# Optimization experiments

Hardware: AMD Instinct MI355X
Metric: run time of the kernel (lower is better)

The kernel has to match this reference:

```python
import jax, jax.numpy as jnp
import numpy as np
import math

B, S, D, H = 2, 2048, 1024, 16
DK = D // H


def setup_inputs() -> dict:
    key = jax.random.key(0)
    ks = jax.random.split(key, 12)
    std = 1.0 / math.sqrt(D)
    inp = {
        "query": jax.random.normal(ks[0], (B, S, D), jnp.float32),
        "key_": jax.random.normal(ks[1], (B, S, D), jnp.float32),
        "value": jax.random.normal(ks[2], (B, S, D), jnp.float32),
        # causal mask: True = masked out
        "attn_mask": jnp.triu(jnp.ones((S, S), jnp.bool_), k=1),
        "w_q": jax.random.uniform(ks[3], (D, D), jnp.float32, -std, std),
        "b_q": jax.random.uniform(ks[4], (D,), jnp.float32, -std, std),
        "w_k": jax.random.uniform(ks[5], (D, D), jnp.float32, -std, std),
        "b_k": jax.random.uniform(ks[6], (D,), jnp.float32, -std, std),
        "w_v": jax.random.uniform(ks[7], (D, D), jnp.float32, -std, std),
        "b_v": jax.random.uniform(ks[8], (D,), jnp.float32, -std, std),
        "w_o": jax.random.uniform(ks[9], (D, D), jnp.float32, -std, std),
        "b_o": jax.random.uniform(ks[10], (D,), jnp.float32, -std, std),
    }
    return inp


def reference(query, key_, value, attn_mask, w_q, b_q, w_k, b_k, w_v, b_v, w_o, b_o):
    # linear projections (torch Linear: x @ W.T + b)
    q = query @ w_q.T + b_q
    k = key_ @ w_k.T + b_k
    v = value @ w_v.T + b_v
    # [B, H, S, DK]
    q = q.reshape(B, S, H, DK).transpose(0, 2, 1, 3)
    k = k.reshape(B, S, H, DK).transpose(0, 2, 1, 3)
    v = v.reshape(B, S, H, DK).transpose(0, 2, 1, 3)
    scores = jnp.einsum("bhqd,bhkd->bhqk", q, k) / jnp.sqrt(jnp.float32(DK))
    scores = jnp.where(attn_mask[None, None, :, :], -jnp.inf, scores)
    attn = jax.nn.softmax(scores, axis=-1)
    context = jnp.einsum("bhqk,bhkd->bhqd", attn, v)
    context = context.transpose(0, 2, 1, 3).reshape(B, S, D)
    return context @ w_o.T + b_o
```

## Files before the change

kernel.cpp:

```cpp
#include <hip/hip_runtime.h>

#define B_ 2
#define S_ 2048
#define D_ 1024
#define H_ 16
#define DK_ 64
#define K_ 1024

typedef __bf16 bf16x8 __attribute__((ext_vector_type(8)));
typedef __bf16 bf16x4 __attribute__((ext_vector_type(4)));
typedef float f32x4 __attribute__((ext_vector_type(4)));

#define QSCALE 0.18033688011112042f

__device__ __forceinline__ void gload16(const void* g, void* l) {
    __builtin_amdgcn_global_load_lds(
        (const __attribute__((address_space(1))) unsigned int*)g,
        (__attribute__((address_space(3))) unsigned int*)l, 16, 0, 0);
}

__device__ __forceinline__ bf16x8 cvt8f(const float* __restrict__ p) {
    f32x4 a = *reinterpret_cast<const f32x4*>(p);
    f32x4 b = *reinterpret_cast<const f32x4*>(p + 4);
    bf16x8 r;
#pragma unroll
    for (int j = 0; j < 4; ++j) { r[j] = (__bf16)a[j]; r[j + 4] = (__bf16)b[j]; }
    return r;
}

__global__ __launch_bounds__(256) void cvt_all(
    const float* __restrict__ s0, const float* __restrict__ s1, const float* __restrict__ s2,
    const float* __restrict__ s3, const float* __restrict__ s4, const float* __restrict__ s5,
    const float* __restrict__ s6,
    __bf16* __restrict__ d0, __bf16* __restrict__ d1, __bf16* __restrict__ d2,
    __bf16* __restrict__ d3, __bf16* __restrict__ d4, __bf16* __restrict__ d5,
    __bf16* __restrict__ d6)
{
    const int y = blockIdx.y;
    const float* s; __bf16* d; int n8;
    const int n8_big = (B_ * S_ * D_) / 8, n8_w = (D_ * D_) / 8;
    switch (y) {
        case 0: s = s0; d = d0; n8 = n8_big; break;
        case 1: s = s1; d = d1; n8 = n8_big; break;
        case 2: s = s2; d = d2; n8 = n8_big; break;
        case 3: s = s3; d = d3; n8 = n8_w; break;
        case 4: s = s4; d = d4; n8 = n8_w; break;
        case 5: s = s5; d = d5; n8 = n8_w; break;
        default: s = s6; d = d6; n8 = n8_w; break;
    }
    int i = blockIdx.x * 256 + threadIdx.x;
    if (i >= n8) return;
    *reinterpret_cast<bf16x8*>(d + (size_t)i * 8) = cvt8f(s + (size_t)i * 8);
}

__global__ __launch_bounds__(512, 2) void gemm_qkv8(
    const __bf16* __restrict__ qin, const __bf16* __restrict__ kin, const __bf16* __restrict__ vin,
    const __bf16* __restrict__ wq,  const __bf16* __restrict__ wk,  const __bf16* __restrict__ wv,
    const float* __restrict__ bq,   const float* __restrict__ bk,   const float* __restrict__ bv,
    __bf16* __restrict__ qo, __bf16* __restrict__ ko, __bf16* __restrict__ vto)
{
    __shared__ __attribute__((aligned(128))) char lds[8 * 16384];

    const int tid = threadIdx.x;
    const int w = tid >> 6, lane = tid & 63;
    const int l15 = lane & 15, lh = lane >> 4;
    const int wr = w >> 2, wc = w & 3;

    const int wg   = blockIdx.x;
    const int wgid = (wg & 7) * 24 + (wg >> 3);
    const int z    = wgid >> 6;
    const int rem  = wgid & 63;

    const __bf16* A; const __bf16* Bm;
    if (z == 0)      { A = qin; Bm = wq; }
    else if (z == 1) { A = kin; Bm = wk; }
    else             { A = wv;  Bm = vin; }
    int brow, bcol;
    if (z < 2) { brow = (rem & 15) * 256; bcol = (rem >> 4) * 256; }
    else       { brow = (rem & 3)  * 256; bcol = (rem >> 2) * 256; }

    const char* Ab = (const char*)A;
    const char* Bb = (const char*)Bm;
    const int abase = brow * 2048;
    const int bbase = bcol * 2048;

    int soff[2];
#pragma unroll
    for (int j = 0; j < 2; ++j) {
        const int s = j * 512 + tid;
        const int row = s >> 2, cslot = s & 3;
        const int cswz = cslot ^ (((row >> 3) & 1) << 1);
        soff[j] = row * 2048 + cswz * 16;
    }

    auto stageHT = [&](int g, int slot) {
        const int u = g >> 2, kind = g & 3;
        const char* src = (kind & 1) ? Bb : Ab;
        const int base = ((kind & 1) ? bbase : abase) + u * 128 + (kind >> 1) * 64;
#pragma unroll
        for (int j = 0; j < 2; ++j) {
            const int ldst = __builtin_amdgcn_readfirstlane(slot * 16384 + j * 8192 + w * 1024);
            gload16(src + (size_t)(base + soff[j]), (char*)lds + ldst);
        }
    };

    const int ainner = (l15 * 64 + lh * 16) ^ ((l15 & 8) << 2);

    f32x4 acc[8][4] = {};
    bf16x8 bfr[4];

    stageHT(0, 0); stageHT(1, 1); stageHT(2, 2);
    stageHT(3, 3); stageHT(4, 4); stageHT(5, 5);
    asm volatile("s_waitcnt vmcnt(8)" ::: "memory");
    __builtin_amdgcn_s_barrier();

#define PHASE(PAR, KS, MH, RDB, P)                                                   \
    {                                                                                \
        bf16x8 af[4];                                                                \
        _Pragma("unroll")                                                            \
        for (int q = 0; q < 4; ++q)                                                  \
            af[q] = *reinterpret_cast<const bf16x8*>(                                \
                lds + ((PAR) * 4 + (KS) * 2) * 16384 + (wr * 8 + (MH) * 4 + q) * 1024 + ainner); \
        if (RDB) {                                                                   \
            _Pragma("unroll")                                                        \
            for (int q = 0; q < 4; ++q)                                              \
                bfr[q] = *reinterpret_cast<const bf16x8*>(                           \
                    lds + ((PAR) * 4 + (KS) * 2 + 1) * 16384 + (wc * 4 + q) * 1024 + ainner); \
        }                                                                            \
        { const int g = 8 * i + 6 + (P); if (g < 64) stageHT(g, (6 + (P)) & 7); }    \
        __builtin_amdgcn_s_barrier();                                                \
        asm volatile("s_waitcnt lgkmcnt(0)" ::: "memory");                           \
        __builtin_amdgcn_sched_barrier(0);                                           \
        __builtin_amdgcn_s_setprio(1);                                               \
        _Pragma("unroll")                                                            \
        for (int q = 0; q < 4; ++q)                                                  \
            _Pragma("unroll")                                                        \
            for (int n = 0; n < 4; ++n)                                              \
                acc[(MH) * 4 + q][n] = __builtin_amdgcn_mfma_f32_16x16x32_bf16(      \
                    bfr[n], af[q], acc[(MH) * 4 + q][n], 0, 0, 0);                   \
        __builtin_amdgcn_s_setprio(0);                                               \
    }

    for (int i = 0; i < 8; ++i) {
        const bool last = (i == 7);
        PHASE(0, 0, 0, 1, 0);
        __builtin_amdgcn_s_barrier();
        PHASE(0, 0, 1, 0, 1);
        asm volatile("s_waitcnt vmcnt(6)" ::: "memory");
        __builtin_amdgcn_s_barrier();
        PHASE(0, 1, 0, 1, 2);
        __builtin_amdgcn_s_barrier();
        PHASE(0, 1, 1, 0, 3);
        if (!last) { asm volatile("s_waitcnt vmcnt(6)" ::: "memory"); }
        else       { asm volatile("s_waitcnt vmcnt(4)" ::: "memory"); }
        __builtin_amdgcn_s_barrier();
        PHASE(1, 0, 0, 1, 4);
        __builtin_amdgcn_s_barrier();
        PHASE(1, 0, 1, 0, 5);
        if (!last) { asm volatile("s_waitcnt vmcnt(6)" ::: "memory"); }
        else       { asm volatile("s_waitcnt vmcnt(0)" ::: "memory"); }
        __builtin_amdgcn_s_barrier();
        PHASE(1, 1, 0, 1, 6);
        __builtin_amdgcn_s_barrier();
        PHASE(1, 1, 1, 0, 7);
        if (!last) {
            asm volatile("s_waitcnt vmcnt(6)" ::: "memory");
            __builtin_amdgcn_s_barrier();
        }
    }
#undef PHASE

    if (z < 2) {
        const float* bias = (z == 0) ? bq : bk;
        __bf16* o = (z == 0) ? qo : ko;
#pragma unroll
        for (int ni = 0; ni < 4; ++ni) {
            const int n4  = bcol + wc * 64 + ni * 16 + lh * 4;
            const f32x4 b4 = *reinterpret_cast<const f32x4*>(bias + n4);
            const int hh = n4 >> 6, dk4 = n4 & 63;
#pragma unroll
            for (int mi = 0; mi < 8; ++mi) {
                const int m  = brow + wr * 128 + mi * 16 + l15;
                const int bb = m >> 11, ss = m & (S_ - 1);
                bf16x4 pk;
#pragma unroll
                for (int r = 0; r < 4; ++r) {
                    float v = acc[mi][ni][r] + b4[r];
                    if (z == 0) v *= QSCALE;
                    pk[r] = (__bf16)v;
                }
                *reinterpret_cast<bf16x4*>(
                    o + (((size_t)(bb * H_ + hh)) * S_ + ss) * DK_ + dk4) = pk;
            }
        }
    } else {
#pragma unroll
        for (int mi = 0; mi < 8; ++mi) {
            const int m  = brow + wr * 128 + mi * 16 + l15;
            const int hh = m >> 6, dk = m & 63;
            const float bias = bv[m];
#pragma unroll
            for (int ni = 0; ni < 4; ++ni) {
                const int n4 = bcol + wc * 64 + ni * 16 + lh * 4;
                const int bb = n4 >> 11, ss = n4 & (S_ - 1);
                bf16x4 pk;
#pragma unroll
                for (int r = 0; r < 4; ++r)
                    pk[r] = (__bf16)(acc[mi][ni][r] + bias);
                *reinterpret_cast<bf16x4*>(
                    vto + (((size_t)(bb * H_ + hh)) * DK_ + dk) * S_ + ss) = pk;
            }
        }
    }
}

__global__ __launch_bounds__(256) void gemm_out(
    const __bf16* __restrict__ A, const __bf16* __restrict__ Bm,
    const float* __restrict__ bias, float* __restrict__ out)
{
    __shared__ __attribute__((aligned(16))) __bf16 ldsA[2 * 128 * 32];
    __shared__ __attribute__((aligned(16))) __bf16 ldsB[2 * 128 * 32];

    const int wg   = blockIdx.x;
    const int wgid = (wg & 7) * 32 + (wg >> 3);
    const int by   = wgid >> 5;
    const int bx   = wgid & 31;
    const int brow = bx * 128;
    const int bcol = by * 128;

    const int tid = threadIdx.x;
    const int w = tid >> 6, lane = tid & 63;
    const int l15 = lane & 15, lh = lane >> 4;
    const int wr = w >> 1, wc = w & 1;
    const int srow  = lane >> 2;
    const int scolb = (((lane & 3) ^ ((lane >> 3) & 3))) * 16;
    const char* Ab = (const char*)A;
    const char* Bb = (const char*)Bm;

    auto stage = [&](int buf, int k0) {
#pragma unroll
        for (int c = 0; c < 2; ++c) {
            const int chunk = w * 2 + c;
            const int row   = chunk * 16 + srow;
            const int loff  = __builtin_amdgcn_readfirstlane(buf * 8192 + chunk * 1024);
            gload16(Ab + (size_t)(brow + row) * 2048 + k0 * 2 + scolb, (char*)ldsA + loff);
            gload16(Bb + (size_t)(bcol + row) * 2048 + k0 * 2 + scolb, (char*)ldsB + loff);
        }
    };

    const int rsw = ((l15 >> 1) & 3);

    f32x4 acc[4][4] = {};
    stage(0, 0);
    int buf = 0;
    for (int k0 = 0; k0 < K_; k0 += 32) {
        if (k0 + 32 < K_) {
            stage(buf ^ 1, k0 + 32);
            asm volatile("s_waitcnt vmcnt(4)" ::: "memory");
        } else {
            asm volatile("s_waitcnt vmcnt(0)" ::: "memory");
        }
        __builtin_amdgcn_s_barrier();
        __builtin_amdgcn_sched_barrier(0);

        const int bo = buf * 8192;
        bf16x8 af[4], bfr[4];
#pragma unroll
        for (int m = 0; m < 4; ++m) {
            const int row = wr * 64 + m * 16 + l15;
            af[m] = *reinterpret_cast<const bf16x8*>(
                (const char*)ldsA + bo + row * 64 + ((lh ^ rsw) * 16));
        }
#pragma unroll
        for (int n = 0; n < 4; ++n) {
            const int row = wc * 64 + n * 16 + l15;
            bfr[n] = *reinterpret_cast<const bf16x8*>(
                (const char*)ldsB + bo + row * 64 + ((lh ^ rsw) * 16));
        }

        __builtin_amdgcn_s_setprio(1);
#pragma unroll
        for (int m = 0; m < 4; ++m)
#pragma unroll
            for (int n = 0; n < 4; ++n)
                acc[m][n] = __builtin_amdgcn_mfma_f32_16x16x32_bf16(bfr[n], af[m], acc[m][n], 0, 0, 0);
        __builtin_amdgcn_s_setprio(0);

        __builtin_amdgcn_s_barrier();
        buf ^= 1;
    }

#pragma unroll
    for (int ni = 0; ni < 4; ++ni) {
        const int n4 = bcol + wc * 64 + ni * 16 + lh * 4;
        const f32x4 b4 = *reinterpret_cast<const f32x4*>(bias + n4);
#pragma unroll
        for (int mi = 0; mi < 4; ++mi) {
            const int m = brow + wr * 64 + mi * 16 + l15;
            f32x4 v;
#pragma unroll
            for (int r = 0; r < 4; ++r) v[r] = acc[mi][ni][r] + b4[r];
            *reinterpret_cast<f32x4*>(out + (size_t)m * D_ + n4) = v;
        }
    }
}

__global__ __launch_bounds__(256, 4) void attn_kernel(
    const __bf16* __restrict__ Q, const __bf16* __restrict__ K,
    const __bf16* __restrict__ VT, __bf16* __restrict__ CTX)
{
    __shared__ __attribute__((aligned(16))) char ldsK[2][8192];
    __shared__ __attribute__((aligned(16))) char ldsV[2][8192];
    __shared__ __attribute__((aligned(16))) __bf16 p_lds[4][16][64];

    const int tid = threadIdx.x;
    const int w = tid >> 6, l = tid & 63;
    const int l15 = l & 15, lh = l >> 4;

    const int c  = blockIdx.x & 255;
    const int rr = blockIdx.x >> 8;
    const int qq = c >> 5;
    const int bhidx = c & 31;
    int panel;
    if (rr == 0)      panel = 31 - qq;
    else if (rr == 1) panel = qq;
    else if (rr == 2) panel = 23 - qq;
    else              panel = 8 + qq;
    const int h = bhidx & 15;
    const int b = bhidx >> 4;

    const size_t bh = (size_t)(b * H_ + h);
    const __bf16* qp   = Q + bh * S_ * DK_;
    const char*  kbase = (const char*)(K  + bh * S_ * DK_);
    const char*  vbase = (const char*)(VT + bh * DK_ * S_);

    const int np = panel + 1;
    const int wave_base = panel * 64 + w * 16;

    const int srow = l >> 3;
    const int ssw  = ((l & 7) * 16) ^ (srow * 16);

    auto stage = [&](int pos) {
        const int k0 = pos * 64;
        char* lk = ldsK[pos & 1];
        char* lv = ldsV[pos & 1];
#pragma unroll
        for (int i = 0; i < 2; ++i) {
            const int r0   = w * 16 + i * 8;
            const int loff = __builtin_amdgcn_readfirstlane(r0 * 128);
            gload16(kbase + (size_t)(k0 + r0 + srow) * 128 + ssw, lk + loff);
            gload16(vbase + (size_t)(r0 + srow) * 4096 + (size_t)k0 * 2 + ssw, lv + loff);
        }
    };

    bf16x8 aq[2];
#pragma unroll
    for (int cc = 0; cc < 2; ++cc)
        aq[cc] = *reinterpret_cast<const bf16x8*>(
            qp + (size_t)(wave_base + l15) * DK_ + cc * 32 + lh * 8);

    bf16x8 vones;
#pragma unroll
    for (int j = 0; j < 8; ++j) vones[j] = (__bf16)1.0f;
    const f32x4 fzero = {0.f, 0.f, 0.f, 0.f};

    f32x4 acc[4] = {};
    f32x4 acc_l = {};
    float mrun = -INFINITY;

    stage(0);

    for (int it = 0; it < np; ++it) {
        if (it + 1 < np) {
            stage(it + 1);
            asm volatile("s_waitcnt vmcnt(4)" ::: "memory");
        } else {
            asm volatile("s_waitcnt vmcnt(0)" ::: "memory");
        }
        __builtin_amdgcn_s_barrier();
        __builtin_amdgcn_sched_barrier(0);

        const int k0 = it * 64;
        const char* lk = ldsK[it & 1];
        const char* lv = ldsV[it & 1];

        bf16x8 ak[4][2];
#pragma unroll
        for (int t = 0; t < 4; ++t)
#pragma unroll
            for (int cc = 0; cc < 2; ++cc) {
                const int col = (cc * 64 + lh * 16) ^ ((l15 & 7) << 4);
                ak[t][cc] = *reinterpret_cast<const bf16x8*>(lk + (t * 16 + l15) * 128 + col);
            }

        f32x4 sacc[4];
        __builtin_amdgcn_s_setprio(1);
#pragma unroll
        for (int t = 0; t < 4; ++t) {
            sacc[t] = __builtin_amdgcn_mfma_f32_16x16x32_bf16(ak[t][0], aq[0], fzero, 0, 0, 0);
            sacc[t] = __builtin_amdgcn_mfma_f32_16x16x32_bf16(ak[t][1], aq[1], sacc[t], 0, 0, 0);
        }
        __builtin_amdgcn_s_setprio(0);

        bf16x8 bv[4][2];
#pragma unroll
        for (int nt = 0; nt < 4; ++nt)
#pragma unroll
            for (int c2 = 0; c2 < 2; ++c2) {
                const int col = (c2 * 64 + lh * 16) ^ ((l15 & 7) << 4);
                bv[nt][c2] = *reinterpret_cast<const bf16x8*>(lv + (nt * 16 + l15) * 128 + col);
            }

        if (k0 + 63 > wave_base) {
            const int qa = wave_base + l15;
#pragma unroll
            for (int t = 0; t < 4; ++t)
#pragma unroll
                for (int r = 0; r < 4; ++r) {
                    const int ka = k0 + t * 16 + lh * 4 + r;
                    if (ka > qa) sacc[t][r] = -INFINITY;
                }
        }

        f32x4 m4 = sacc[0];
#pragma unroll
        for (int t = 1; t < 4; ++t)
#pragma unroll
            for (int r = 0; r < 4; ++r) m4[r] = fmaxf(m4[r], sacc[t][r]);
        float rm = fmaxf(fmaxf(m4[0], m4[1]), fmaxf(m4[2], m4[3]));
        rm = fmaxf(rm, __shfl_xor(rm, 16, 64));
        rm = fmaxf(rm, __shfl_xor(rm, 32, 64));

        if (!__all(rm <= mrun + 8.f)) {
            const float mnew = fmaxf(mrun, rm);
            const float scl  = exp2f(mrun - mnew);
            mrun = mnew;
#pragma unroll
            for (int r = 0; r < 4; ++r) {
                const float sr = __shfl(scl, lh * 4 + r, 64);
#pragma unroll
                for (int nt = 0; nt < 4; ++nt) acc[nt][r] *= sr;
                acc_l[r] *= sr;
            }
        }

#pragma unroll
        for (int t = 0; t < 4; ++t) {
            bf16x4 pk;
#pragma unroll
            for (int r = 0; r < 4; ++r)
                pk[r] = (__bf16)exp2f(sacc[t][r] - mrun);
            const int wcol = (t * 16 + lh * 4) ^ ((l15 & 7) << 3);
            *reinterpret_cast<bf16x4*>(&p_lds[w][l15][wcol]) = pk;
        }

        bf16x8 pa[2];
#pragma unroll
        for (int c2 = 0; c2 < 2; ++c2) {
            const int rcol = (c2 * 32 + lh * 8) ^ ((l15 & 7) << 3);
            pa[c2] = *reinterpret_cast<const bf16x8*>(&p_lds[w][l15][rcol]);
        }

        __builtin_amdgcn_s_setprio(1);
#pragma unroll
        for (int nt = 0; nt < 4; ++nt)
#pragma unroll
            for (int c2 = 0; c2 < 2; ++c2)
                acc[nt] = __builtin_amdgcn_mfma_f32_16x16x32_bf16(
                    pa[c2], bv[nt][c2], acc[nt], 0, 0, 0);
        acc_l = __builtin_amdgcn_mfma_f32_16x16x32_bf16(pa[0], vones, acc_l, 0, 0, 0);
        acc_l = __builtin_amdgcn_mfma_f32_16x16x32_bf16(pa[1], vones, acc_l, 0, 0, 0);
        __builtin_amdgcn_s_setprio(0);

        __builtin_amdgcn_s_barrier();
    }

#pragma unroll
    for (int r = 0; r < 4; ++r) {
        const float linv = 1.f / acc_l[r];
        const int srow2 = wave_base + lh * 4 + r;
#pragma unroll
        for (int nt = 0; nt < 4; ++nt)
            CTX[((size_t)b * S_ + srow2) * D_ + h * DK_ + nt * 16 + l15] =
                (__bf16)(acc[nt][r] * linv);
    }
}

extern "C" void kernel_launch(void* const* d_in, const int* in_sizes, int n_in,
                              void* d_out, int out_size, void* d_ws, size_t ws_size,
                              hipStream_t stream) {
    (void)in_sizes; (void)n_in; (void)out_size; (void)ws_size;

    const float* query = (const float*)d_in[0];
    const float* key_  = (const float*)d_in[1];
    const float* value = (const float*)d_in[2];
    const float* w_q = (const float*)d_in[4];
    const float* b_q = (const float*)d_in[5];
    const float* w_k = (const float*)d_in[6];
    const float* b_k = (const float*)d_in[7];
    const float* w_v = (const float*)d_in[8];
    const float* b_v = (const float*)d_in[9];
    const float* w_o = (const float*)d_in[10];
    const float* b_o = (const float*)d_in[11];
    float* out = (float*)d_out;

    char* Wp = (char*)d_ws;
    const size_t MB = 1024 * 1024;
    __bf16* qin = (__bf16*)(Wp + 0 * MB);
    __bf16* kin = (__bf16*)(Wp + 8 * MB);
    __bf16* vin = (__bf16*)(Wp + 16 * MB);
    __bf16* wq  = (__bf16*)(Wp + 24 * MB);
    __bf16* wk  = (__bf16*)(Wp + 26 * MB);
    __bf16* wv  = (__bf16*)(Wp + 28 * MB);
    __bf16* wo  = (__bf16*)(Wp + 30 * MB);
    __bf16* q   = (__bf16*)(Wp + 32 * MB);
    __bf16* k   = (__bf16*)(Wp + 40 * MB);
    __bf16* vt  = (__bf16*)(Wp + 48 * MB);
    __bf16* ctx = qin;

    const int n8_big = (B_ * S_ * D_) / 8;

    hipLaunchKernelGGL(cvt_all, dim3(n8_big / (256 * 8) * 8, 7), dim3(256), 0, stream,
                       query, key_, value, w_q, w_k, w_v, w_o,
                       qin, kin, vin, wq, wk, wv, wo);
    hipLaunchKernelGGL(gemm_qkv8, dim3(192), dim3(512), 0, stream,
                       qin, kin, vin, wq, wk, wv, b_q, b_k, b_v, q, k, vt);
    hipLaunchKernelGGL(attn_kernel, dim3(1024), dim3(256), 0, stream,
                       q, k, vt, ctx);
    hipLaunchKernelGGL(gemm_out, dim3(256), dim3(256), 0, stream,
                       ctx, wo, b_o, out);
}
```

Measured before the change: 119.9 us.

## Pair high and low causal query panels per block to share K/V tiles

Each attention block now handles two query panels, panel 31-pi and panel pi, so the grid becomes 512 blocks. The K/V tiles staged into LDS for the long panel are reused by the short panel during its first iterations, which balances causal work across blocks and cuts redundant K/V loads. In exchange it doubles the accumulator registers, so launch bounds drop from 4 to 3 blocks per CU, and there are fewer blocks in flight.

```diff
diff --git a/kernel.cpp b/kernel.cpp
--- a/kernel.cpp
+++ b/kernel.cpp
@@ -305,27 +305,21 @@
     }
 }
 
-__global__ __launch_bounds__(256, 4) void attn_kernel(
+__global__ __launch_bounds__(256, 3) void attn_kernel(
     const __bf16* __restrict__ Q, const __bf16* __restrict__ K,
     const __bf16* __restrict__ VT, __bf16* __restrict__ CTX)
 {
     __shared__ __attribute__((aligned(16))) char ldsK[2][8192];
     __shared__ __attribute__((aligned(16))) char ldsV[2][8192];
-    __shared__ __attribute__((aligned(16))) __bf16 p_lds[4][16][64];
+    __shared__ __attribute__((aligned(16))) __bf16 p_lds[4][2][16][64];
 
     const int tid = threadIdx.x;
     const int w = tid >> 6, l = tid & 63;
     const int l15 = l & 15, lh = l >> 4;
 
-    const int c  = blockIdx.x & 255;
-    const int rr = blockIdx.x >> 8;
-    const int qq = c >> 5;
-    const int bhidx = c & 31;
-    int panel;
-    if (rr == 0)      panel = 31 - qq;
-    else if (rr == 1) panel = qq;
-    else if (rr == 2) panel = 23 - qq;
-    else              panel = 8 + qq;
+    const int pi    = blockIdx.x >> 5;
+    const int bhidx = blockIdx.x & 31;
+    const int ph    = 31 - pi;
     const int h = bhidx & 15;
     const int b = bhidx >> 4;
 
@@ -334,8 +328,9 @@
     const char*  kbase = (const char*)(K  + bh * S_ * DK_);
     const char*  vbase = (const char*)(VT + bh * DK_ * S_);
 
-    const int np = panel + 1;
-    const int wave_base = panel * 64 + w * 16;
+    const int NT  = ph + 1;
+    const int wbH = ph * 64 + w * 16;
+    const int wbL = pi * 64 + w * 16;
 
     const int srow = l >> 3;
     const int ssw  = ((l & 7) * 16) ^ (srow * 16);
@@ -353,25 +348,28 @@
         }
     };
 
-    bf16x8 aq[2];
-#pragma unroll
-    for (int cc = 0; cc < 2; ++cc)
-        aq[cc] = *reinterpret_cast<const bf16x8*>(
-            qp + (size_t)(wave_base + l15) * DK_ + cc * 32 + lh * 8);
+    bf16x8 aqH[2], aqL[2];
+#pragma unroll
+    for (int cc = 0; cc < 2; ++cc) {
+        aqH[cc] = *reinterpret_cast<const bf16x8*>(
+            qp + (size_t)(wbH + l15) * DK_ + cc * 32 + lh * 8);
+        aqL[cc] = *reinterpret_cast<const bf16x8*>(
+            qp + (size_t)(wbL + l15) * DK_ + cc * 32 + lh * 8);
+    }
 
     bf16x8 vones;
 #pragma unroll
     for (int j = 0; j < 8; ++j) vones[j] = (__bf16)1.0f;
     const f32x4 fzero = {0.f, 0.f, 0.f, 0.f};
 
-    f32x4 acc[4] = {};
-    f32x4 acc_l = {};
-    float mrun = -INFINITY;
+    f32x4 accH[4] = {}, accL[4] = {};
+    f32x4 aclH = {}, aclL = {};
+    float mrunH = -INFINITY, mrunL = -INFINITY;
 
     stage(0);
 
-    for (int it = 0; it < np; ++it) {
-        if (it + 1 < np) {
+    for (int it = 0; it < NT; ++it) {
+        if (it + 1 < NT) {
             stage(it + 1);
             asm volatile("s_waitcnt vmcnt(4)" ::: "memory");
         } else {
@@ -383,6 +381,7 @@
         const int k0 = it * 64;
         const char* lk = ldsK[it & 1];
         const char* lv = ldsV[it & 1];
+        const bool lact = (it <= pi);
 
         bf16x8 ak[4][2];
 #pragma unroll
@@ -393,12 +392,19 @@
                 ak[t][cc] = *reinterpret_cast<const bf16x8*>(lk + (t * 16 + l15) * 128 + col);
             }
 
-        f32x4 sacc[4];
+        f32x4 saccH[4], saccL[4];
         __builtin_amdgcn_s_setprio(1);
 #pragma unroll
         for (int t = 0; t < 4; ++t) {
-            sacc[t] = __builtin_amdgcn_mfma_f32_16x16x32_bf16(ak[t][0], aq[0], fzero, 0, 0, 0);
-            sacc[t] = __builtin_amdgcn_mfma_f32_16x16x32_bf16(ak[t][1], aq[1], sacc[t], 0, 0, 0);
+            saccH[t] = __builtin_amdgcn_mfma_f32_16x16x32_bf16(ak[t][0], aqH[0], fzero, 0, 0, 0);
+            saccH[t] = __builtin_amdgcn_mfma_f32_16x16x32_bf16(ak[t][1], aqH[1], saccH[t], 0, 0, 0);
+        }
+        if (lact) {
+#pragma unroll
+            for (int t = 0; t < 4; ++t) {
+                saccL[t] = __builtin_amdgcn_mfma_f32_16x16x32_bf16(ak[t][0], aqL[0], fzero, 0, 0, 0);
+                saccL[t] = __builtin_amdgcn_mfma_f32_16x16x32_bf16(ak[t][1], aqL[1], saccL[t], 0, 0, 0);
+            }
         }
         __builtin_amdgcn_s_setprio(0);
 
@@ -411,78 +417,138 @@
                 bv[nt][c2] = *reinterpret_cast<const bf16x8*>(lv + (nt * 16 + l15) * 128 + col);
             }
 
-        if (k0 + 63 > wave_base) {
-            const int qa = wave_base + l15;
+        if (k0 + 63 > wbH) {
+            const int qa = wbH + l15;
 #pragma unroll
             for (int t = 0; t < 4; ++t)
 #pragma unroll
                 for (int r = 0; r < 4; ++r) {
                     const int ka = k0 + t * 16 + lh * 4 + r;
-                    if (ka > qa) sacc[t][r] = -INFINITY;
+                    if (ka > qa) saccH[t][r] = -INFINITY;
                 }
         }
-
-        f32x4 m4 = sacc[0];
-#pragma unroll
-        for (int t = 1; t < 4; ++t)
-#pragma unroll
-            for (int r = 0; r < 4; ++r) m4[r] = fmaxf(m4[r], sacc[t][r]);
-        float rm = fmaxf(fmaxf(m4[0], m4[1]), fmaxf(m4[2], m4[3]));
-        rm = fmaxf(rm, __shfl_xor(rm, 16, 64));
-        rm = fmaxf(rm, __shfl_xor(rm, 32, 64));
-
-        if (!__all(rm <= mrun + 8.f)) {
-            const float mnew = fmaxf(mrun, rm);
-            const float scl  = exp2f(mrun - mnew);
-            mrun = mnew;
-#pragma unroll
-            for (int r = 0; r < 4; ++r) {
-                const float sr = __shfl(scl, lh * 4 + r, 64);
-#pragma unroll
-                for (int nt = 0; nt < 4; ++nt) acc[nt][r] *= sr;
-                acc_l[r] *= sr;
-            }
-        }
-
-#pragma unroll
-        for (int t = 0; t < 4; ++t) {
-            bf16x4 pk;
-#pragma unroll
-            for (int r = 0; r < 4; ++r)
-                pk[r] = (__bf16)exp2f(sacc[t][r] - mrun);
-            const int wcol = (t * 16 + lh * 4) ^ ((l15 & 7) << 3);
-            *reinterpret_cast<bf16x4*>(&p_lds[w][l15][wcol]) = pk;
-        }
-
-        bf16x8 pa[2];
-#pragma unroll
-        for (int c2 = 0; c2 < 2; ++c2) {
-            const int rcol = (c2 * 32 + lh * 8) ^ ((l15 & 7) << 3);
-            pa[c2] = *reinterpret_cast<const bf16x8*>(&p_lds[w][l15][rcol]);
-        }
-
-        __builtin_amdgcn_s_setprio(1);
-#pragma unroll
-        for (int nt = 0; nt < 4; ++nt)
-#pragma unroll
-            for (int c2 = 0; c2 < 2; ++c2)
-                acc[nt] = __builtin_amdgcn_mfma_f32_16x16x32_bf16(
-                    pa[c2], bv[nt][c2], acc[nt], 0, 0, 0);
-        acc_l = __builtin_amdgcn_mfma_f32_16x16x32_bf16(pa[0], vones, acc_l, 0, 0, 0);
-        acc_l = __builtin_amdgcn_mfma_f32_16x16x32_bf16(pa[1], vones, acc_l, 0, 0, 0);
-        __builtin_amdgcn_s_setprio(0);
+        {
+            f32x4 m4 = saccH[0];
+#pragma unroll
+            for (int t = 1; t < 4; ++t)
+#pragma unroll
+                for (int r = 0; r < 4; ++r) m4[r] = fmaxf(m4[r], saccH[t][r]);
+            float rm = fmaxf(fmaxf(m4[0], m4[1]), fmaxf(m4[2], m4[3]));
+            rm = fmaxf(rm, __shfl_xor(rm, 16, 64));
+            rm = fmaxf(rm, __shfl_xor(rm, 32, 64));
+            if (!__all(rm <= mrunH + 8.f)) {
+                const float mnew = fmaxf(mrunH, rm);
+                const float scl  = exp2f(mrunH - mnew);
+                mrunH = mnew;
+#pragma unroll
+                for (int r = 0; r < 4; ++r) {
+                    const float sr = __shfl(scl, lh * 4 + r, 64);
+#pragma unroll
+                    for (int nt = 0; nt < 4; ++nt) accH[nt][r] *= sr;
+                    aclH[r] *= sr;
+                }
+            }
+#pragma unroll
+            for (int t = 0; t < 4; ++t) {
+                bf16x4 pk;
+#pragma unroll
+                for (int r = 0; r < 4; ++r)
+                    pk[r] = (__bf16)exp2f(saccH[t][r] - mrunH);
+                const int wcol = (t * 16 + lh * 4) ^ ((l15 & 7) << 3);
+                *reinterpret_cast<bf16x4*>(&p_lds[w][0][l15][wcol]) = pk;
+            }
+            bf16x8 pa[2];
+#pragma unroll
+            for (int c2 = 0; c2 < 2; ++c2) {
+                const int rcol = (c2 * 32 + lh * 8) ^ ((l15 & 7) << 3);
+                pa[c2] = *reinterpret_cast<const bf16x8*>(&p_lds[w][0][l15][rcol]);
+            }
+            __builtin_amdgcn_s_setprio(1);
+#pragma unroll
+            for (int nt = 0; nt < 4; ++nt)
+#pragma unroll
+                for (int c2 = 0; c2 < 2; ++c2)
+                    accH[nt] = __builtin_amdgcn_mfma_f32_16x16x32_bf16(
+                        pa[c2], bv[nt][c2], accH[nt], 0, 0, 0);
+            aclH = __builtin_amdgcn_mfma_f32_16x16x32_bf16(pa[0], vones, aclH, 0, 0, 0);
+            aclH = __builtin_amdgcn_mfma_f32_16x16x32_bf16(pa[1], vones, aclH, 0, 0, 0);
+            __builtin_amdgcn_s_setprio(0);
+        }
+
+        if (lact) {
+            if (k0 + 63 > wbL) {
+                const int qa = wbL + l15;
+#pragma unroll
+                for (int t = 0; t < 4; ++t)
+#pragma unroll
+                    for (int r = 0; r < 4; ++r) {
+                        const int ka = k0 + t * 16 + lh * 4 + r;
+                        if (ka > qa) saccL[t][r] = -INFINITY;
+                    }
+            }
+            f32x4 m4 = saccL[0];
+#pragma unroll
+            for (int t = 1; t < 4; ++t)
+#pragma unroll
+                for (int r = 0; r < 4; ++r) m4[r] = fmaxf(m4[r], saccL[t][r]);
+            float rm = fmaxf(fmaxf(m4[0], m4[1]), fmaxf(m4[2], m4[3]));
+            rm = fmaxf(rm, __shfl_xor(rm, 16, 64));
+            rm = fmaxf(rm, __shfl_xor(rm, 32, 64));
+            if (!__all(rm <= mrunL + 8.f)) {
+                const float mnew = fmaxf(mrunL, rm);
+                const float scl  = exp2f(mrunL - mnew);
+                mrunL = mnew;
+#pragma unroll
+                for (int r = 0; r < 4; ++r) {
+                    const float sr = __shfl(scl, lh * 4 + r, 64);
+#pragma unroll
+                    for (int nt = 0; nt < 4; ++nt) accL[nt][r] *= sr;
+                    aclL[r] *= sr;
+                }
+            }
+#pragma unroll
+            for (int t = 0; t < 4; ++t) {
+                bf16x4 pk;
+#pragma unroll
+                for (int r = 0; r < 4; ++r)
+                    pk[r] = (__bf16)exp2f(saccL[t][r] - mrunL);
+                const int wcol = (t * 16 + lh * 4) ^ ((l15 & 7) << 3);
+                *reinterpret_cast<bf16x4*>(&p_lds[w][1][l15][wcol]) = pk;
+            }
+            bf16x8 pa[2];
+#pragma unroll
+            for (int c2 = 0; c2 < 2; ++c2) {
+                const int rcol = (c2 * 32 + lh * 8) ^ ((l15 & 7) << 3);
+                pa[c2] = *reinterpret_cast<const bf16x8*>(&p_lds[w][1][l15][rcol]);
+            }
+            __builtin_amdgcn_s_setprio(1);
+#pragma unroll
+            for (int nt = 0; nt < 4; ++nt)
+#pragma unroll
+                for (int c2 = 0; c2 < 2; ++c2)
+                    accL[nt] = __builtin_amdgcn_mfma_f32_16x16x32_bf16(
+                        pa[c2], bv[nt][c2], accL[nt], 0, 0, 0);
+            aclL = __builtin_amdgcn_mfma_f32_16x16x32_bf16(pa[0], vones, aclL, 0, 0, 0);
+            aclL = __builtin_amdgcn_mfma_f32_16x16x32_bf16(pa[1], vones, aclL, 0, 0, 0);
+            __builtin_amdgcn_s_setprio(0);
+        }
 
         __builtin_amdgcn_s_barrier();
     }
 
 #pragma unroll
     for (int r = 0; r < 4; ++r) {
-        const float linv = 1.f / acc_l[r];
-        const int srow2 = wave_base + lh * 4 + r;
-#pragma unroll
-        for (int nt = 0; nt < 4; ++nt)
-            CTX[((size_t)b * S_ + srow2) * D_ + h * DK_ + nt * 16 + l15] =
-                (__bf16)(acc[nt][r] * linv);
+        const float linvH = 1.f / aclH[r];
+        const float linvL = 1.f / aclL[r];
+        const int sH = wbH + lh * 4 + r;
+        const int sL = wbL + lh * 4 + r;
+#pragma unroll
+        for (int nt = 0; nt < 4; ++nt) {
+            CTX[((size_t)b * S_ + sH) * D_ + h * DK_ + nt * 16 + l15] =
+                (__bf16)(accH[nt][r] * linvH);
+            CTX[((size_t)b * S_ + sL) * D_ + h * DK_ + nt * 16 + l15] =
+                (__bf16)(accL[nt][r] * linvL);
+        }
     }
 }
 
@@ -525,7 +591,7 @@
                        qin, kin, vin, wq, wk, wv, wo);
     hipLaunchKernelGGL(gemm_qkv8, dim3(192), dim3(512), 0, stream,
                        qin, kin, vin, wq, wk, wv, b_q, b_k, b_v, q, k, vt);
-    hipLaunchKernelGGL(attn_kernel, dim3(1024), dim3(256), 0, stream,
+    hipLaunchKernelGGL(attn_kernel, dim3(512), dim3(256), 0, stream,
                        q, k, vt, ctx);
     hipLaunchKernelGGL(gemm_out, dim3(256), dim3(256), 0, stream,
                        ctx, wo, b_o, out);
```

New measurement: 120.8 us. About the same (+0.8%).
